# Optimization experiments

Measured on AMD Instinct MI355X. Metric: run time of the kernel, lower is better.

Reference implementation:

```python
import jax, jax.numpy as jnp
import numpy as np

E = 8
H = 1024
I = 2816
T = 4096
INIT_STD = 0.02
# Fixed ragged group sizes (tokens per expert), sum == T. Tokens are assumed
# pre-sorted by expert, as in the original grouped-GEMM dispatch.
GROUP_SIZES = np.array([256, 1024, 128, 512, 768, 384, 640, 384], dtype=np.int32)
assert GROUP_SIZES.sum() == T


def setup_inputs() -> dict:
    key = jax.random.key(0)
    k_x, k1, k2, k3 = jax.random.split(key, 4)
    hidden_states = jax.random.normal(k_x, (T, H), dtype=jnp.float32)
    w1 = jax.random.normal(k1, (E, H, I), dtype=jnp.float32) * INIT_STD  # up proj
    w2 = jax.random.normal(k2, (E, I, H), dtype=jnp.float32) * INIT_STD  # down proj
    w3 = jax.random.normal(k3, (E, H, I), dtype=jnp.float32) * INIT_STD  # gate proj
    group_sizes = jnp.asarray(GROUP_SIZES)
    return {"hidden_states": hidden_states, "group_sizes": group_sizes,
            "w1": w1, "w2": w2, "w3": w3}


def reference(hidden_states, group_sizes, w1, w2, w3):
    """Grouped SwiGLU expert FFN: out = w2[e] @ (silu(w1[e] x) * (w3[e] x))
    where expert e owns a contiguous ragged slice of tokens given by group_sizes.
    """
    n_exp = w1.shape[0]
    n_tok = hidden_states.shape[0]
    # per-token expert id from ragged group sizes (tokens sorted by expert)
    seg = jnp.repeat(jnp.arange(n_exp), group_sizes, total_repeat_length=n_tok)  # [T]
    out = jnp.zeros((n_tok, w2.shape[2]), dtype=hidden_states.dtype)
    for e in range(n_exp):  # small fixed expert count
        m = (seg == e)[:, None]
        xe = jnp.where(m, hidden_states, 0.0)                       # [T,H] masked
        h = jax.nn.silu(xe @ w1[e]) * (xe @ w3[e])                  # [T,I] SwiGLU
        out = out + jnp.where(m, h @ w2[e], 0.0)                    # [T,H]
    return out
```

## Files before the change

kernel.cpp:

```cpp
#include <hip/hip_runtime.h>
#include <hip/hip_bf16.h>

#define TOK 4096
#define HD  1024
#define ID  2816

typedef __bf16 bf16_t;
typedef bf16_t bf16x4 __attribute__((ext_vector_type(4)));
typedef bf16_t bf16x8 __attribute__((ext_vector_type(8)));
typedef float  f32x4  __attribute__((ext_vector_type(4)));
typedef float  f32x16 __attribute__((ext_vector_type(16)));

__constant__ int tile_expert[32] = {
  0,0, 1,1,1,1,1,1,1,1, 2, 3,3,3,3, 4,4,4,4,4,4, 5,5,5, 6,6,6,6,6, 7,7,7
};

__constant__ int xcd_mtiles[32] = {
   2, 3, 4, 5,
   6, 7, 8, 9,
  11,12,13,14,
  15,16,17,18,
  24,25,26,27,
  10,21,22,23,
  28,29,30,31,
   0, 1,19,20
};

__device__ __forceinline__ int swz64(int r, int c) {
    return (r << 6) + (((c ^ r ^ (r >> 2)) & 3) << 4);
}
__device__ __forceinline__ int swz128(int r, int c) {
    return (r << 7) + (((c ^ r) & 7) << 4);
}

__global__ __launch_bounds__(256, 8)
void cast_x(const float* __restrict__ X, bf16_t* __restrict__ Xb)
{
    const int i = (blockIdx.x * 256 + threadIdx.x) * 8;
    f32x4 a = *(const f32x4*)(X + i);
    f32x4 b = *(const f32x4*)(X + i + 4);
    bf16x8 o;
    #pragma unroll
    for (int t = 0; t < 4; ++t) { o[t] = (bf16_t)a[t]; o[4 + t] = (bf16_t)b[t]; }
    *(bf16x8*)(Xb + i) = o;
}

__global__ __launch_bounds__(256, 4)
void gemm_up_fused(const bf16_t* __restrict__ Xb, const float* __restrict__ W1,
                   const float* __restrict__ W3, bf16_t* __restrict__ Hbuf)
{
    __shared__ __align__(16) char Xs[2][8192];
    __shared__ __align__(16) char Us[2][4096];
    __shared__ __align__(16) char Gs[2][4096];

    const int lin   = blockIdx.x + (blockIdx.y << 5);
    const int xcd   = lin & 7;
    const int ii    = lin >> 3;
    const int mtile = xcd_mtiles[(xcd << 2) | (ii / 44)];
    const int ntile = ii % 44;
    const int e  = tile_expert[mtile];
    const int m0 = mtile << 7;
    const int n0 = ntile << 6;

    const int tid  = threadIdx.x;
    const int lane = tid & 63;
    const int wid  = tid >> 6;
    const int wm = (wid >> 1) << 6;
    const int wn = (wid & 1) << 5;
    const int lr = lane & 31;
    const int lh = lane >> 5;

    const int ar = tid >> 1, ah = tid & 1;
    const int wsel = tid >> 7;
    const int t7 = tid & 127;
    const int wa = t7 >> 4;
    const int wb = t7 & 15;

    const bf16_t* asrc = Xb + (size_t)(m0 + ar) * HD + ah * 16;
    const float*  wsrc = (wsel ? W3 : W1) + (size_t)e * HD * ID
                       + (size_t)(wa * 4) * ID + n0 + wb * 4;

    f32x16 accu[2] = {};
    f32x16 accg[2] = {};
    bf16x8 av[2];
    f32x4  wv[4];

    auto LOAD = [&]() {
        av[0] = *(const bf16x8*)(asrc);
        av[1] = *(const bf16x8*)(asrc + 8);
        #pragma unroll
        for (int i2 = 0; i2 < 4; ++i2) wv[i2] = *(const f32x4*)(wsrc + (size_t)i2 * ID);
        asrc += 32;
        wsrc += (size_t)32 * ID;
    };
    auto STORE = [&](int buf) {
        char* xb = Xs[buf];
        *(bf16x8*)(xb + swz64(ar, ah * 2 + 0)) = av[0];
        *(bf16x8*)(xb + swz64(ar, ah * 2 + 1)) = av[1];
        char* wdst = wsel ? Gs[buf] : Us[buf];
        #pragma unroll
        for (int jj = 0; jj < 4; ++jj) {
            bf16x4 b;
            #pragma unroll
            for (int i2 = 0; i2 < 4; ++i2) b[i2] = (bf16_t)wv[i2][jj];
            const int row = wb * 4 + jj;
            *(bf16x4*)(wdst + (row << 6)
                       + ((((wa >> 1) ^ row ^ (row >> 2)) & 3) << 4)
                       + ((wa & 1) << 3)) = b;
        }
    };
    auto COMPUTE = [&](int buf) {
        const char* xb = Xs[buf];
        const char* ub = Us[buf];
        const char* gb = Gs[buf];
        #pragma unroll
        for (int ksub = 0; ksub < 2; ++ksub) {
            const int c = ksub * 2 + lh;
            bf16x8 a0 = *(const bf16x8*)(xb + swz64(wm + lr,      c));
            bf16x8 a1 = *(const bf16x8*)(xb + swz64(wm + 32 + lr, c));
            bf16x8 u  = *(const bf16x8*)(ub + swz64(wn + lr,      c));
            bf16x8 g  = *(const bf16x8*)(gb + swz64(wn + lr,      c));
            accu[0] = __builtin_amdgcn_mfma_f32_32x32x16_bf16(a0, u, accu[0], 0, 0, 0);
            accu[1] = __builtin_amdgcn_mfma_f32_32x32x16_bf16(a1, u, accu[1], 0, 0, 0);
            accg[0] = __builtin_amdgcn_mfma_f32_32x32x16_bf16(a0, g, accg[0], 0, 0, 0);
            accg[1] = __builtin_amdgcn_mfma_f32_32x32x16_bf16(a1, g, accg[1], 0, 0, 0);
        }
    };

    LOAD();
    STORE(0);
    __syncthreads();
    for (int ks = 0; ks < HD / 32 - 1; ++ks) {
        LOAD();
        COMPUTE(ks & 1);
        STORE((ks + 1) & 1);
        __syncthreads();
    }
    COMPUTE((HD / 32 - 1) & 1);

    const int orow = m0 + wm + (lh << 2);
    const int ocol = n0 + wn + lr;
    #pragma unroll
    for (int mf = 0; mf < 2; ++mf) {
        #pragma unroll
        for (int r = 0; r < 16; ++r) {
            const int row = orow + mf * 32 + (r & 3) + ((r >> 2) << 3);
            float u = accu[mf][r];
            float g = accg[mf][r];
            Hbuf[(size_t)row * ID + ocol] = (bf16_t)(u / (1.0f + __expf(-u)) * g);
        }
    }
}

__global__ __launch_bounds__(256, 3)
void gemm2_down(const bf16_t* __restrict__ Hin, const float* __restrict__ W2,
                float* __restrict__ Out)
{
    __shared__ __align__(16) char Hs [2][16384];
    __shared__ __align__(16) char W2s[2][8192];

    const int lin   = blockIdx.x + (blockIdx.y << 5);
    const int xcd   = lin & 7;
    const int i     = lin >> 3;
    const int mtile = (xcd << 2) | (i & 3);
    const int ntile = i >> 2;
    const int e  = tile_expert[mtile];
    const int m0 = mtile << 7;
    const int n0 = ntile << 6;

    const int tid  = threadIdx.x;
    const int lane = tid & 63;
    const int wid  = tid >> 6;
    const int wm = (wid >> 1) << 6;
    const int wn = (wid & 1) << 5;
    const int lr = lane & 31;
    const int lh = lane >> 5;

    const int hr = tid >> 1, hh = tid & 1;
    const int wa = tid >> 4, wb = tid & 15;

    const bf16_t* hsrc  = Hin + (size_t)(m0 + hr) * ID + hh * 32;
    const float*  w2src = W2 + (size_t)e * ID * HD + (size_t)(wa * 4) * HD + n0 + wb * 4;

    f32x16 acc[2] = {};
    bf16x8 hv[4];
    f32x4  wv[4];

    auto LOAD = [&]() {
        #pragma unroll
        for (int j = 0; j < 4; ++j) hv[j] = *(const bf16x8*)(hsrc + j * 8);
        #pragma unroll
        for (int i2 = 0; i2 < 4; ++i2) wv[i2] = *(const f32x4*)(w2src + (size_t)i2 * HD);
        hsrc  += 64;
        w2src += (size_t)64 * HD;
    };
    auto STORE = [&](int buf) {
        char* hb = Hs[buf];
        #pragma unroll
        for (int j = 0; j < 4; ++j)
            *(bf16x8*)(hb + swz128(hr, hh * 4 + j)) = hv[j];
        char* wdst = W2s[buf];
        #pragma unroll
        for (int jj = 0; jj < 4; ++jj) {
            bf16x4 b;
            #pragma unroll
            for (int i2 = 0; i2 < 4; ++i2) b[i2] = (bf16_t)wv[i2][jj];
            const int row = wb * 4 + jj;
            *(bf16x4*)(wdst + (row << 7)
                       + ((((wa >> 1) ^ row) & 7) << 4)
                       + ((wa & 1) << 3)) = b;
        }
    };
    auto COMPUTE = [&](int buf) {
        const char* hb = Hs[buf];
        const char* wbuf = W2s[buf];
        #pragma unroll
        for (int ksub = 0; ksub < 4; ++ksub) {
            const int c = ksub * 2 + lh;
            bf16x8 a0 = *(const bf16x8*)(hb + swz128(wm + lr,      c));
            bf16x8 a1 = *(const bf16x8*)(hb + swz128(wm + 32 + lr, c));
            bf16x8 b0 = *(const bf16x8*)(wbuf + swz128(wn + lr,    c));
            acc[0] = __builtin_amdgcn_mfma_f32_32x32x16_bf16(a0, b0, acc[0], 0, 0, 0);
            acc[1] = __builtin_amdgcn_mfma_f32_32x32x16_bf16(a1, b0, acc[1], 0, 0, 0);
        }
    };

    LOAD();
    STORE(0);
    __syncthreads();
    for (int ks = 0; ks < ID / 64 - 1; ++ks) {
        LOAD();
        COMPUTE(ks & 1);
        STORE((ks + 1) & 1);
        __syncthreads();
    }
    COMPUTE((ID / 64 - 1) & 1);

    const int orow = m0 + wm + (lh << 2);
    const int ocol = n0 + wn + lr;
    #pragma unroll
    for (int mf = 0; mf < 2; ++mf) {
        #pragma unroll
        for (int r = 0; r < 16; ++r) {
            const int row = orow + mf * 32 + (r & 3) + ((r >> 2) << 3);
            Out[(size_t)row * HD + ocol] = acc[mf][r];
        }
    }
}

extern "C" void kernel_launch(void* const* d_in, const int* in_sizes, int n_in,
                              void* d_out, int out_size, void* d_ws, size_t ws_size,
                              hipStream_t stream)
{
    (void)in_sizes; (void)n_in; (void)out_size; (void)ws_size;
    const float* X  = (const float*)d_in[0];
    const float* W1 = (const float*)d_in[2];
    const float* W2 = (const float*)d_in[3];
    const float* W3 = (const float*)d_in[4];
    float* Out = (float*)d_out;

    bf16_t* Xb   = (bf16_t*)d_ws;
    bf16_t* Hbuf = (bf16_t*)d_ws + (size_t)TOK * HD;

    cast_x<<<dim3(TOK * HD / (256 * 8)), 256, 0, stream>>>(X, Xb);
    gemm_up_fused<<<dim3(TOK / 128, ID / 64), 256, 0, stream>>>(Xb, W1, W3, Hbuf);
    gemm2_down<<<dim3(TOK / 128, HD / 64), 256, 0, stream>>>(Hbuf, W2, Out);
}
```

Baseline: 193.2 us.

## Split fused up/gate GEMM into two launches with wider N tiles

Replaces the fused W1/W3 up-projection kernel with a templated single-weight GEMM launched twice. The first pass writes silu(x·W1) to the hidden buffer and the second multiplies x·W3 into it in place. Each launch uses 128-wide N tiles so every B fragment is reused across two M fragments. The swizzle gains an extra XOR term for the wider tile. The cost is an extra read and write of the bf16 hidden buffer, X being loaded twice, and one more kernel launch.

```diff
diff --git a/kernel.cpp b/kernel.cpp
--- a/kernel.cpp
+++ b/kernel.cpp
@@ -27,7 +27,7 @@
 };
 
 __device__ __forceinline__ int swz64(int r, int c) {
-    return (r << 6) + (((c ^ r ^ (r >> 2)) & 3) << 4);
+    return (r << 6) + (((c ^ r ^ (r >> 2) ^ (r >> 4)) & 3) << 4);
 }
 __device__ __forceinline__ int swz128(int r, int c) {
     return (r << 7) + (((c ^ r) & 7) << 4);
@@ -45,43 +45,38 @@
     *(bf16x8*)(Xb + i) = o;
 }
 
-__global__ __launch_bounds__(256, 4)
-void gemm_up_fused(const bf16_t* __restrict__ Xb, const float* __restrict__ W1,
-                   const float* __restrict__ W3, bf16_t* __restrict__ Hbuf)
+template<int MODE>
+__global__ __launch_bounds__(256, 3)
+void gemm_up(const bf16_t* __restrict__ Xb, const float* __restrict__ W,
+             bf16_t* __restrict__ Hbuf)
 {
     __shared__ __align__(16) char Xs[2][8192];
-    __shared__ __align__(16) char Us[2][4096];
-    __shared__ __align__(16) char Gs[2][4096];
+    __shared__ __align__(16) char Ws[2][8192];
 
     const int lin   = blockIdx.x + (blockIdx.y << 5);
     const int xcd   = lin & 7;
     const int ii    = lin >> 3;
-    const int mtile = xcd_mtiles[(xcd << 2) | (ii / 44)];
-    const int ntile = ii % 44;
+    const int mtile = xcd_mtiles[(xcd << 2) | (ii / 22)];
+    const int ntile = ii % 22;
     const int e  = tile_expert[mtile];
     const int m0 = mtile << 7;
-    const int n0 = ntile << 6;
+    const int n0 = ntile << 7;
 
     const int tid  = threadIdx.x;
     const int lane = tid & 63;
     const int wid  = tid >> 6;
     const int wm = (wid >> 1) << 6;
-    const int wn = (wid & 1) << 5;
+    const int wn = (wid & 1) << 6;
     const int lr = lane & 31;
     const int lh = lane >> 5;
 
     const int ar = tid >> 1, ah = tid & 1;
-    const int wsel = tid >> 7;
-    const int t7 = tid & 127;
-    const int wa = t7 >> 4;
-    const int wb = t7 & 15;
+    const int wa = tid >> 5, wb = tid & 31;
 
     const bf16_t* asrc = Xb + (size_t)(m0 + ar) * HD + ah * 16;
-    const float*  wsrc = (wsel ? W3 : W1) + (size_t)e * HD * ID
-                       + (size_t)(wa * 4) * ID + n0 + wb * 4;
-
-    f32x16 accu[2] = {};
-    f32x16 accg[2] = {};
+    const float*  wsrc = W + (size_t)e * HD * ID + (size_t)(wa * 4) * ID + n0 + wb * 4;
+
+    f32x16 acc[2][2] = {};
     bf16x8 av[2];
     f32x4  wv[4];
 
@@ -97,33 +92,32 @@
         char* xb = Xs[buf];
         *(bf16x8*)(xb + swz64(ar, ah * 2 + 0)) = av[0];
         *(bf16x8*)(xb + swz64(ar, ah * 2 + 1)) = av[1];
-        char* wdst = wsel ? Gs[buf] : Us[buf];
-        #pragma unroll
-        for (int jj = 0; jj < 4; ++jj) {
+        char* wd = Ws[buf];
+        #pragma unroll
+        for (int j = 0; j < 4; ++j) {
             bf16x4 b;
             #pragma unroll
-            for (int i2 = 0; i2 < 4; ++i2) b[i2] = (bf16_t)wv[i2][jj];
-            const int row = wb * 4 + jj;
-            *(bf16x4*)(wdst + (row << 6)
-                       + ((((wa >> 1) ^ row ^ (row >> 2)) & 3) << 4)
+            for (int i2 = 0; i2 < 4; ++i2) b[i2] = (bf16_t)wv[i2][j];
+            const int n = wb * 4 + j;
+            *(bf16x4*)(wd + (n << 6)
+                       + ((((wa >> 1) ^ n ^ (n >> 2) ^ (n >> 4)) & 3) << 4)
                        + ((wa & 1) << 3)) = b;
         }
     };
     auto COMPUTE = [&](int buf) {
         const char* xb = Xs[buf];
-        const char* ub = Us[buf];
-        const char* gb = Gs[buf];
+        const char* wbuf = Ws[buf];
         #pragma unroll
         for (int ksub = 0; ksub < 2; ++ksub) {
             const int c = ksub * 2 + lh;
             bf16x8 a0 = *(const bf16x8*)(xb + swz64(wm + lr,      c));
             bf16x8 a1 = *(const bf16x8*)(xb + swz64(wm + 32 + lr, c));
-            bf16x8 u  = *(const bf16x8*)(ub + swz64(wn + lr,      c));
-            bf16x8 g  = *(const bf16x8*)(gb + swz64(wn + lr,      c));
-            accu[0] = __builtin_amdgcn_mfma_f32_32x32x16_bf16(a0, u, accu[0], 0, 0, 0);
-            accu[1] = __builtin_amdgcn_mfma_f32_32x32x16_bf16(a1, u, accu[1], 0, 0, 0);
-            accg[0] = __builtin_amdgcn_mfma_f32_32x32x16_bf16(a0, g, accg[0], 0, 0, 0);
-            accg[1] = __builtin_amdgcn_mfma_f32_32x32x16_bf16(a1, g, accg[1], 0, 0, 0);
+            bf16x8 b0 = *(const bf16x8*)(wbuf + swz64(wn + lr,      c));
+            bf16x8 b1 = *(const bf16x8*)(wbuf + swz64(wn + 32 + lr, c));
+            acc[0][0] = __builtin_amdgcn_mfma_f32_32x32x16_bf16(a0, b0, acc[0][0], 0, 0, 0);
+            acc[0][1] = __builtin_amdgcn_mfma_f32_32x32x16_bf16(a0, b1, acc[0][1], 0, 0, 0);
+            acc[1][0] = __builtin_amdgcn_mfma_f32_32x32x16_bf16(a1, b0, acc[1][0], 0, 0, 0);
+            acc[1][1] = __builtin_amdgcn_mfma_f32_32x32x16_bf16(a1, b1, acc[1][1], 0, 0, 0);
         }
     };
 
@@ -143,11 +137,20 @@
     #pragma unroll
     for (int mf = 0; mf < 2; ++mf) {
         #pragma unroll
-        for (int r = 0; r < 16; ++r) {
-            const int row = orow + mf * 32 + (r & 3) + ((r >> 2) << 3);
-            float u = accu[mf][r];
-            float g = accg[mf][r];
-            Hbuf[(size_t)row * ID + ocol] = (bf16_t)(u / (1.0f + __expf(-u)) * g);
+        for (int nf = 0; nf < 2; ++nf) {
+            #pragma unroll
+            for (int r = 0; r < 16; ++r) {
+                const int row = orow + mf * 32 + (r & 3) + ((r >> 2) << 3);
+                const int col = ocol + nf * 32;
+                bf16_t* p = Hbuf + (size_t)row * ID + col;
+                float v = acc[mf][nf][r];
+                if (MODE == 0) {
+                    *p = (bf16_t)(v / (1.0f + __expf(-v)));
+                } else {
+                    float s = (float)(*p);
+                    *p = (bf16_t)(s * v);
+                }
+            }
         }
     }
 }
@@ -263,6 +266,7 @@
     bf16_t* Hbuf = (bf16_t*)d_ws + (size_t)TOK * HD;
 
     cast_x<<<dim3(TOK * HD / (256 * 8)), 256, 0, stream>>>(X, Xb);
-    gemm_up_fused<<<dim3(TOK / 128, ID / 64), 256, 0, stream>>>(Xb, W1, W3, Hbuf);
+    gemm_up<0><<<dim3(32, ID / 128), 256, 0, stream>>>(Xb, W1, Hbuf);
+    gemm_up<1><<<dim3(32, ID / 128), 256, 0, stream>>>(Xb, W3, Hbuf);
     gemm2_down<<<dim3(TOK / 128, HD / 64), 256, 0, stream>>>(Hbuf, W2, Out);
 }
```

Result: slower. 211.2 us (+9.3%).
